# Kernel tuning notes

Measured on AMD Instinct MI355X. Metric: run time of the kernel, lower is better.

## Reference

```python
import jax, jax.numpy as jnp
import numpy as np

B, S, R, H = 256, 196, 1024, 512  # batch, att regions, rnn_size, att_hid_size


def setup_inputs() -> dict:
    key = jax.random.key(0)
    ks = jax.random.split(key, 8)
    return {
        "att_feats": jax.random.normal(ks[0], (B, S, R), dtype=jnp.float32),
        "p_att_feats": jax.random.normal(ks[1], (B, S, H), dtype=jnp.float32),
        "hidden": jax.random.normal(ks[2], (B, R), dtype=jnp.float32),
        "in_weights": jax.random.uniform(ks[3], (B, S), dtype=jnp.float32),
        "h2att_w": jax.random.normal(ks[4], (H, R), dtype=jnp.float32) * (1.0 / np.sqrt(R)),
        "h2att_b": jnp.full((H,), 0.1, dtype=jnp.float32),
        "alpha_w": jax.random.normal(ks[5], (1, H), dtype=jnp.float32) * (1.0 / np.sqrt(H)),
        "alpha_b": jnp.full((1,), 0.1, dtype=jnp.float32),
    }


def reference(att_feats, p_att_feats, hidden, in_weights, h2att_w, h2att_b, alpha_w, alpha_b):
    # att = in_weights * p_att_feats          [B, S, H]
    att = in_weights[:, :, None] * p_att_feats
    # att_h = h2att(hidden)                   [B, H] broadcast over S
    att_h = hidden @ h2att_w.T + h2att_b
    dot = jnp.tanh(att + att_h[:, None, :])   # [B, S, H]
    # alpha_net: Linear(H, 1) -> scores       [B, S]
    scores = jnp.einsum('bsh,h->bs', dot, alpha_w[0]) + alpha_b[0]
    weight = jax.nn.softmax(scores, axis=-1)  # [B, S]
    # weighted pooling: bmm(weight[:,None,:], att_feats).squeeze(1)
    att_res = jnp.einsum('bs,bsr->br', weight, att_feats)  # [B, R]
    return (att_res, weight)
```

## Files before the change

kernel.cpp:

```cpp
#include <hip/hip_runtime.h>
#include <math.h>

#define BN 256
#define SN 196
#define RN 1024
#define HN 512
#define KSPLIT 16
#define KCH 64

__device__ __forceinline__ float fast_tanh(float x) {
    float e = __expf(2.0f * x);
    return 1.0f - 2.0f * __builtin_amdgcn_rcpf(e + 1.0f);
}

__global__ __launch_bounds__(256) void k_gemm_partial(
    const float* __restrict__ hidden, const float* __restrict__ w,
    float* __restrict__ partial) {
    __shared__ float At[KCH][64];
    __shared__ float Bt[KCH][64];
    const int t  = threadIdx.x;
    const int b0 = blockIdx.x * 64;
    const int h0 = blockIdx.y * 64;
    const int kc = blockIdx.z;
    const int k0 = kc * KCH;

    {
        const int row = t >> 2, kq = (t & 3) * 16;
        const float* srcA = hidden + (size_t)(b0 + row) * RN + k0 + kq;
        const float* srcB = w      + (size_t)(h0 + row) * RN + k0 + kq;
#pragma unroll
        for (int j = 0; j < 4; ++j) {
            float4 v = *(const float4*)(srcA + j * 4);
            int k = kq + j * 4;
            At[k][row] = v.x; At[k + 1][row] = v.y; At[k + 2][row] = v.z; At[k + 3][row] = v.w;
        }
#pragma unroll
        for (int j = 0; j < 4; ++j) {
            float4 v = *(const float4*)(srcB + j * 4);
            int k = kq + j * 4;
            Bt[k][row] = v.x; Bt[k + 1][row] = v.y; Bt[k + 2][row] = v.z; Bt[k + 3][row] = v.w;
        }
    }
    __syncthreads();

    const int th4 = (t & 15) * 4;
    const int tb4 = (t >> 4) * 4;
    float4 acc0 = {0,0,0,0}, acc1 = {0,0,0,0}, acc2 = {0,0,0,0}, acc3 = {0,0,0,0};
#pragma unroll 8
    for (int k = 0; k < KCH; ++k) {
        float4 a  = *(const float4*)&At[k][tb4];
        float4 bb = *(const float4*)&Bt[k][th4];
        acc0.x = fmaf(a.x, bb.x, acc0.x); acc0.y = fmaf(a.x, bb.y, acc0.y);
        acc0.z = fmaf(a.x, bb.z, acc0.z); acc0.w = fmaf(a.x, bb.w, acc0.w);
        acc1.x = fmaf(a.y, bb.x, acc1.x); acc1.y = fmaf(a.y, bb.y, acc1.y);
        acc1.z = fmaf(a.y, bb.z, acc1.z); acc1.w = fmaf(a.y, bb.w, acc1.w);
        acc2.x = fmaf(a.z, bb.x, acc2.x); acc2.y = fmaf(a.z, bb.y, acc2.y);
        acc2.z = fmaf(a.z, bb.z, acc2.z); acc2.w = fmaf(a.z, bb.w, acc2.w);
        acc3.x = fmaf(a.w, bb.x, acc3.x); acc3.y = fmaf(a.w, bb.y, acc3.y);
        acc3.z = fmaf(a.w, bb.z, acc3.z); acc3.w = fmaf(a.w, bb.w, acc3.w);
    }
    float* dst = partial + ((size_t)kc * BN + b0 + tb4) * HN + h0 + th4;
    *(float4*)(dst)          = acc0;
    *(float4*)(dst + HN)     = acc1;
    *(float4*)(dst + 2 * HN) = acc2;
    *(float4*)(dst + 3 * HN) = acc3;
}

__global__ __launch_bounds__(1024) void k_fused(
    const float* __restrict__ partial, const float* __restrict__ bias,
    const float* __restrict__ p_att, const float* __restrict__ in_w,
    const float* __restrict__ alpha_w, const float* __restrict__ att_feats,
    float* __restrict__ att_res, float* __restrict__ weight_out) {
    __shared__ float att_h[HN];
    __shared__ float sc[256];
    __shared__ float red[16 * 256];
    const int b    = blockIdx.x;
    const int t    = threadIdx.x;
    const int wv   = t >> 6;
    const int lane = t & 63;

    if (t >= SN && t < 256) sc[t] = -1e30f;

    if (t < 128) {
        float4 s = *(const float4*)(bias + t * 4);
        const float* p = partial + (size_t)b * HN + t * 4;
#pragma unroll
        for (int kc = 0; kc < KSPLIT; ++kc) {
            float4 v = *(const float4*)(p + (size_t)kc * BN * HN);
            s.x += v.x; s.y += v.y; s.z += v.z; s.w += v.w;
        }
        *(float4*)&att_h[t * 4] = s;
    }
    __syncthreads();

    {
        const float4* a4 = (const float4*)alpha_w;
        float4 aw0 = a4[lane], aw1 = a4[lane + 64];
        float4 ah0 = *(const float4*)&att_h[lane * 4];
        float4 ah1 = *(const float4*)&att_h[(lane + 64) * 4];
        const float4* p4 = (const float4*)p_att;
        for (int si = wv; si < SN; si += 16) {
            float  iw = in_w[b * SN + si];
            size_t rb = (size_t)(b * SN + si) * (HN / 4);
            float4 p0 = p4[rb + lane];
            float4 p1 = p4[rb + lane + 64];
            float sum;
            sum  = fast_tanh(fmaf(iw, p0.x, ah0.x)) * aw0.x;
            sum += fast_tanh(fmaf(iw, p0.y, ah0.y)) * aw0.y;
            sum += fast_tanh(fmaf(iw, p0.z, ah0.z)) * aw0.z;
            sum += fast_tanh(fmaf(iw, p0.w, ah0.w)) * aw0.w;
            sum += fast_tanh(fmaf(iw, p1.x, ah1.x)) * aw1.x;
            sum += fast_tanh(fmaf(iw, p1.y, ah1.y)) * aw1.y;
            sum += fast_tanh(fmaf(iw, p1.z, ah1.z)) * aw1.z;
            sum += fast_tanh(fmaf(iw, p1.w, ah1.w)) * aw1.w;
#pragma unroll
            for (int off = 32; off; off >>= 1) sum += __shfl_xor(sum, off, 64);
            if (lane == 0) sc[si] = sum;
        }
    }
    __syncthreads();

    if (wv == 0) {
        float v0 = sc[lane], v1 = sc[lane + 64], v2 = sc[lane + 128], v3 = sc[lane + 192];
        float m = fmaxf(fmaxf(v0, v1), fmaxf(v2, v3));
#pragma unroll
        for (int off = 32; off; off >>= 1) m = fmaxf(m, __shfl_xor(m, off, 64));
        float e0 = __expf(v0 - m), e1 = __expf(v1 - m);
        float e2 = __expf(v2 - m), e3 = __expf(v3 - m);
        float s = e0 + e1 + e2 + e3;
#pragma unroll
        for (int off = 32; off; off >>= 1) s += __shfl_xor(s, off, 64);
        float inv = 1.0f / s;
        e0 *= inv; e1 *= inv; e2 *= inv; e3 *= inv;
        sc[lane] = e0; sc[lane + 64] = e1; sc[lane + 128] = e2; sc[lane + 192] = e3;
        float* wo = weight_out + (size_t)b * SN;
        wo[lane] = e0; wo[lane + 64] = e1; wo[lane + 128] = e2;
        if (lane + 192 < SN) wo[lane + 192] = e3;
    }
    __syncthreads();

    {
        const int g = wv >> 2, q = wv & 3;
        const float* base = att_feats + (size_t)b * SN * RN + q * 256 + lane * 4;
        float4 acc = {0,0,0,0};
        for (int i = 0; i < 49; i += 7) {
#pragma unroll
            for (int j = 0; j < 7; ++j) {
                int s = g + 4 * (i + j);
                float ws = sc[s];
                float4 v = *(const float4*)(base + (size_t)s * RN);
                acc.x = fmaf(ws, v.x, acc.x);
                acc.y = fmaf(ws, v.y, acc.y);
                acc.z = fmaf(ws, v.z, acc.z);
                acc.w = fmaf(ws, v.w, acc.w);
            }
        }
        *(float4*)&red[wv * 256 + lane * 4] = acc;
    }
    __syncthreads();
    {
        const int q2 = t >> 8, rr = t & 255;
        float r = red[q2 * 256 + rr] + red[(4 + q2) * 256 + rr]
                + red[(8 + q2) * 256 + rr] + red[(12 + q2) * 256 + rr];
        att_res[(size_t)b * RN + t] = r;
    }
}

extern "C" void kernel_launch(void* const* d_in, const int* in_sizes, int n_in,
                              void* d_out, int out_size, void* d_ws, size_t ws_size,
                              hipStream_t stream) {
    const float* att_feats   = (const float*)d_in[0];
    const float* p_att_feats = (const float*)d_in[1];
    const float* hidden      = (const float*)d_in[2];
    const float* in_weights  = (const float*)d_in[3];
    const float* h2att_w     = (const float*)d_in[4];
    const float* h2att_b     = (const float*)d_in[5];
    const float* alpha_w     = (const float*)d_in[6];

    float* att_res = (float*)d_out;
    float* weight  = (float*)d_out + BN * RN;
    float* partial = (float*)d_ws;

    k_gemm_partial<<<dim3(BN / 64, HN / 64, KSPLIT), 256, 0, stream>>>(
        hidden, h2att_w, partial);
    k_fused<<<BN, 1024, 0, stream>>>(partial, h2att_b, p_att_feats, in_weights,
                                     alpha_w, att_feats, att_res, weight);
}
```

Baseline: 363.0 us.

## Split fused attention kernel into separate reduce, scores, softmax and pool kernels

Replaces the single per-batch 1024-thread fused kernel with four kernels: a split-K reduction for att_h, a scores kernel with one wave per (batch, region) row, a softmax kernel, and a pooling kernel with two blocks per batch. The GEMM split-K factor is halved, and each GEMM block now loops over two 64-wide K sub-tiles. The aim is to spread the memory-bound p_att and att_feats streaming across many more blocks than the previous 256 large blocks. In exchange it adds kernel launches and round trips through global memory for att_h and the scores, and the pool kernel has only 512 small blocks.

```diff
diff --git a/kernel.cpp b/kernel.cpp
--- a/kernel.cpp
+++ b/kernel.cpp
@@ -5,8 +5,8 @@
 #define SN 196
 #define RN 1024
 #define HN 512
-#define KSPLIT 16
-#define KCH 64
+#define KSPLIT 8
+#define KCH 128
 
 __device__ __forceinline__ float fast_tanh(float x) {
     float e = __expf(2.0f * x);
@@ -16,48 +16,51 @@
 __global__ __launch_bounds__(256) void k_gemm_partial(
     const float* __restrict__ hidden, const float* __restrict__ w,
     float* __restrict__ partial) {
-    __shared__ float At[KCH][64];
-    __shared__ float Bt[KCH][64];
+    __shared__ float At[64][64];
+    __shared__ float Bt[64][64];
     const int t  = threadIdx.x;
     const int b0 = blockIdx.x * 64;
     const int h0 = blockIdx.y * 64;
     const int kc = blockIdx.z;
-    const int k0 = kc * KCH;
-
-    {
-        const int row = t >> 2, kq = (t & 3) * 16;
-        const float* srcA = hidden + (size_t)(b0 + row) * RN + k0 + kq;
-        const float* srcB = w      + (size_t)(h0 + row) * RN + k0 + kq;
-#pragma unroll
-        for (int j = 0; j < 4; ++j) {
-            float4 v = *(const float4*)(srcA + j * 4);
-            int k = kq + j * 4;
-            At[k][row] = v.x; At[k + 1][row] = v.y; At[k + 2][row] = v.z; At[k + 3][row] = v.w;
-        }
-#pragma unroll
-        for (int j = 0; j < 4; ++j) {
-            float4 v = *(const float4*)(srcB + j * 4);
-            int k = kq + j * 4;
-            Bt[k][row] = v.x; Bt[k + 1][row] = v.y; Bt[k + 2][row] = v.z; Bt[k + 3][row] = v.w;
-        }
-    }
-    __syncthreads();
 
     const int th4 = (t & 15) * 4;
     const int tb4 = (t >> 4) * 4;
     float4 acc0 = {0,0,0,0}, acc1 = {0,0,0,0}, acc2 = {0,0,0,0}, acc3 = {0,0,0,0};
+
+    for (int sub = 0; sub < 2; ++sub) {
+        const int k0 = kc * KCH + sub * 64;
+        {
+            const int row = t >> 2, kq = (t & 3) * 16;
+            const float* srcA = hidden + (size_t)(b0 + row) * RN + k0 + kq;
+            const float* srcB = w      + (size_t)(h0 + row) * RN + k0 + kq;
+#pragma unroll
+            for (int j = 0; j < 4; ++j) {
+                float4 v = *(const float4*)(srcA + j * 4);
+                int k = kq + j * 4;
+                At[k][row] = v.x; At[k+1][row] = v.y; At[k+2][row] = v.z; At[k+3][row] = v.w;
+            }
+#pragma unroll
+            for (int j = 0; j < 4; ++j) {
+                float4 v = *(const float4*)(srcB + j * 4);
+                int k = kq + j * 4;
+                Bt[k][row] = v.x; Bt[k+1][row] = v.y; Bt[k+2][row] = v.z; Bt[k+3][row] = v.w;
+            }
+        }
+        __syncthreads();
 #pragma unroll 8
-    for (int k = 0; k < KCH; ++k) {
-        float4 a  = *(const float4*)&At[k][tb4];
-        float4 bb = *(const float4*)&Bt[k][th4];
-        acc0.x = fmaf(a.x, bb.x, acc0.x); acc0.y = fmaf(a.x, bb.y, acc0.y);
-        acc0.z = fmaf(a.x, bb.z, acc0.z); acc0.w = fmaf(a.x, bb.w, acc0.w);
-        acc1.x = fmaf(a.y, bb.x, acc1.x); acc1.y = fmaf(a.y, bb.y, acc1.y);
-        acc1.z = fmaf(a.y, bb.z, acc1.z); acc1.w = fmaf(a.y, bb.w, acc1.w);
-        acc2.x = fmaf(a.z, bb.x, acc2.x); acc2.y = fmaf(a.z, bb.y, acc2.y);
-        acc2.z = fmaf(a.z, bb.z, acc2.z); acc2.w = fmaf(a.z, bb.w, acc2.w);
-        acc3.x = fmaf(a.w, bb.x, acc3.x); acc3.y = fmaf(a.w, bb.y, acc3.y);
-        acc3.z = fmaf(a.w, bb.z, acc3.z); acc3.w = fmaf(a.w, bb.w, acc3.w);
+        for (int k = 0; k < 64; ++k) {
+            float4 a  = *(const float4*)&At[k][tb4];
+            float4 bb = *(const float4*)&Bt[k][th4];
+            acc0.x = fmaf(a.x, bb.x, acc0.x); acc0.y = fmaf(a.x, bb.y, acc0.y);
+            acc0.z = fmaf(a.x, bb.z, acc0.z); acc0.w = fmaf(a.x, bb.w, acc0.w);
+            acc1.x = fmaf(a.y, bb.x, acc1.x); acc1.y = fmaf(a.y, bb.y, acc1.y);
+            acc1.z = fmaf(a.y, bb.z, acc1.z); acc1.w = fmaf(a.y, bb.w, acc1.w);
+            acc2.x = fmaf(a.z, bb.x, acc2.x); acc2.y = fmaf(a.z, bb.y, acc2.y);
+            acc2.z = fmaf(a.z, bb.z, acc2.z); acc2.w = fmaf(a.z, bb.w, acc2.w);
+            acc3.x = fmaf(a.w, bb.x, acc3.x); acc3.y = fmaf(a.w, bb.y, acc3.y);
+            acc3.z = fmaf(a.w, bb.z, acc3.z); acc3.w = fmaf(a.w, bb.w, acc3.w);
+        }
+        __syncthreads();
     }
     float* dst = partial + ((size_t)kc * BN + b0 + tb4) * HN + h0 + th4;
     *(float4*)(dst)          = acc0;
@@ -66,104 +69,111 @@
     *(float4*)(dst + 3 * HN) = acc3;
 }
 
-__global__ __launch_bounds__(1024) void k_fused(
+__global__ __launch_bounds__(128) void k_reduce(
     const float* __restrict__ partial, const float* __restrict__ bias,
+    float* __restrict__ att_h) {
+    const int b = blockIdx.x, t = threadIdx.x;
+    float4 s = *(const float4*)(bias + t * 4);
+    const float* p = partial + (size_t)b * HN + t * 4;
+#pragma unroll
+    for (int kc = 0; kc < KSPLIT; ++kc) {
+        float4 v = *(const float4*)(p + (size_t)kc * BN * HN);
+        s.x += v.x; s.y += v.y; s.z += v.z; s.w += v.w;
+    }
+    *(float4*)(att_h + (size_t)b * HN + t * 4) = s;
+}
+
+__global__ __launch_bounds__(256) void k_scores(
     const float* __restrict__ p_att, const float* __restrict__ in_w,
-    const float* __restrict__ alpha_w, const float* __restrict__ att_feats,
-    float* __restrict__ att_res, float* __restrict__ weight_out) {
-    __shared__ float att_h[HN];
-    __shared__ float sc[256];
-    __shared__ float red[16 * 256];
-    const int b    = blockIdx.x;
+    const float* __restrict__ att_h, const float* __restrict__ alpha_w,
+    float* __restrict__ scores) {
+    const int lane = threadIdx.x & 63;
+    const int gid  = blockIdx.x * 4 + (threadIdx.x >> 6);
+    const int b    = gid / SN;
+
+    const float iw = in_w[gid];
+    const float4* p4 = (const float4*)(p_att + (size_t)gid * HN);
+    const float4* a4 = (const float4*)(alpha_w);
+    const float4* h4 = (const float4*)(att_h + (size_t)b * HN);
+
+    float4 p0 = p4[lane], p1 = p4[lane + 64];
+    float4 aw0 = a4[lane], aw1 = a4[lane + 64];
+    float4 ah0 = h4[lane], ah1 = h4[lane + 64];
+
+    float sum;
+    sum  = fast_tanh(fmaf(iw, p0.x, ah0.x)) * aw0.x;
+    sum += fast_tanh(fmaf(iw, p0.y, ah0.y)) * aw0.y;
+    sum += fast_tanh(fmaf(iw, p0.z, ah0.z)) * aw0.z;
+    sum += fast_tanh(fmaf(iw, p0.w, ah0.w)) * aw0.w;
+    sum += fast_tanh(fmaf(iw, p1.x, ah1.x)) * aw1.x;
+    sum += fast_tanh(fmaf(iw, p1.y, ah1.y)) * aw1.y;
+    sum += fast_tanh(fmaf(iw, p1.z, ah1.z)) * aw1.z;
+    sum += fast_tanh(fmaf(iw, p1.w, ah1.w)) * aw1.w;
+#pragma unroll
+    for (int off = 32; off; off >>= 1) sum += __shfl_xor(sum, off, 64);
+    if (lane == 0) scores[gid] = sum;
+}
+
+__global__ __launch_bounds__(64) void k_softmax(float* __restrict__ wout) {
+    const int b = blockIdx.x, lane = threadIdx.x;
+    float* row = wout + (size_t)b * SN;
+
+    float v[4];
+    float m = -1e30f;
+#pragma unroll
+    for (int i = 0; i < 4; ++i) {
+        int s = lane + i * 64;
+        v[i] = (s < SN) ? row[s] : -1e30f;
+        m = fmaxf(m, v[i]);
+    }
+#pragma unroll
+    for (int off = 32; off; off >>= 1) m = fmaxf(m, __shfl_xor(m, off, 64));
+
+    float e[4];
+    float sum = 0.f;
+#pragma unroll
+    for (int i = 0; i < 4; ++i) {
+        int s = lane + i * 64;
+        e[i] = (s < SN) ? __expf(v[i] - m) : 0.f;
+        sum += e[i];
+    }
+#pragma unroll
+    for (int off = 32; off; off >>= 1) sum += __shfl_xor(sum, off, 64);
+
+    float inv = 1.0f / sum;
+#pragma unroll
+    for (int i = 0; i < 4; ++i) {
+        int s = lane + i * 64;
+        if (s < SN) row[s] = e[i] * inv;
+    }
+}
+
+__global__ __launch_bounds__(128) void k_pool(
+    const float* __restrict__ att_feats, const float* __restrict__ weight,
+    float* __restrict__ att_res) {
+    __shared__ float w[SN];
+    const int b    = blockIdx.x >> 1;
+    const int half = blockIdx.x & 1;
     const int t    = threadIdx.x;
-    const int wv   = t >> 6;
-    const int lane = t & 63;
-
-    if (t >= SN && t < 256) sc[t] = -1e30f;
-
-    if (t < 128) {
-        float4 s = *(const float4*)(bias + t * 4);
-        const float* p = partial + (size_t)b * HN + t * 4;
-#pragma unroll
-        for (int kc = 0; kc < KSPLIT; ++kc) {
-            float4 v = *(const float4*)(p + (size_t)kc * BN * HN);
-            s.x += v.x; s.y += v.y; s.z += v.z; s.w += v.w;
+
+    for (int s = t; s < SN; s += 128) w[s] = weight[(size_t)b * SN + s];
+    __syncthreads();
+
+    const float* base = att_feats + (size_t)b * SN * RN + half * 512 + t * 4;
+    float4 acc = {0, 0, 0, 0};
+    for (int i = 0; i < SN; i += 14) {
+#pragma unroll
+        for (int j = 0; j < 14; ++j) {
+            int s = i + j;
+            float ws = w[s];
+            float4 v = *(const float4*)(base + (size_t)s * RN);
+            acc.x = fmaf(ws, v.x, acc.x);
+            acc.y = fmaf(ws, v.y, acc.y);
+            acc.z = fmaf(ws, v.z, acc.z);
+            acc.w = fmaf(ws, v.w, acc.w);
         }
-        *(float4*)&att_h[t * 4] = s;
-    }
-    __syncthreads();
-
-    {
-        const float4* a4 = (const float4*)alpha_w;
-        float4 aw0 = a4[lane], aw1 = a4[lane + 64];
-        float4 ah0 = *(const float4*)&att_h[lane * 4];
-        float4 ah1 = *(const float4*)&att_h[(lane + 64) * 4];
-        const float4* p4 = (const float4*)p_att;
-        for (int si = wv; si < SN; si += 16) {
-            float  iw = in_w[b * SN + si];
-            size_t rb = (size_t)(b * SN + si) * (HN / 4);
-            float4 p0 = p4[rb + lane];
-            float4 p1 = p4[rb + lane + 64];
-            float sum;
-            sum  = fast_tanh(fmaf(iw, p0.x, ah0.x)) * aw0.x;
-            sum += fast_tanh(fmaf(iw, p0.y, ah0.y)) * aw0.y;
-            sum += fast_tanh(fmaf(iw, p0.z, ah0.z)) * aw0.z;
-            sum += fast_tanh(fmaf(iw, p0.w, ah0.w)) * aw0.w;
-            sum += fast_tanh(fmaf(iw, p1.x, ah1.x)) * aw1.x;
-            sum += fast_tanh(fmaf(iw, p1.y, ah1.y)) * aw1.y;
-            sum += fast_tanh(fmaf(iw, p1.z, ah1.z)) * aw1.z;
-            sum += fast_tanh(fmaf(iw, p1.w, ah1.w)) * aw1.w;
-#pragma unroll
-            for (int off = 32; off; off >>= 1) sum += __shfl_xor(sum, off, 64);
-            if (lane == 0) sc[si] = sum;
-        }
-    }
-    __syncthreads();
-
-    if (wv == 0) {
-        float v0 = sc[lane], v1 = sc[lane + 64], v2 = sc[lane + 128], v3 = sc[lane + 192];
-        float m = fmaxf(fmaxf(v0, v1), fmaxf(v2, v3));
-#pragma unroll
-        for (int off = 32; off; off >>= 1) m = fmaxf(m, __shfl_xor(m, off, 64));
-        float e0 = __expf(v0 - m), e1 = __expf(v1 - m);
-        float e2 = __expf(v2 - m), e3 = __expf(v3 - m);
-        float s = e0 + e1 + e2 + e3;
-#pragma unroll
-        for (int off = 32; off; off >>= 1) s += __shfl_xor(s, off, 64);
-        float inv = 1.0f / s;
-        e0 *= inv; e1 *= inv; e2 *= inv; e3 *= inv;
-        sc[lane] = e0; sc[lane + 64] = e1; sc[lane + 128] = e2; sc[lane + 192] = e3;
-        float* wo = weight_out + (size_t)b * SN;
-        wo[lane] = e0; wo[lane + 64] = e1; wo[lane + 128] = e2;
-        if (lane + 192 < SN) wo[lane + 192] = e3;
-    }
-    __syncthreads();
-
-    {
-        const int g = wv >> 2, q = wv & 3;
-        const float* base = att_feats + (size_t)b * SN * RN + q * 256 + lane * 4;
-        float4 acc = {0,0,0,0};
-        for (int i = 0; i < 49; i += 7) {
-#pragma unroll
-            for (int j = 0; j < 7; ++j) {
-                int s = g + 4 * (i + j);
-                float ws = sc[s];
-                float4 v = *(const float4*)(base + (size_t)s * RN);
-                acc.x = fmaf(ws, v.x, acc.x);
-                acc.y = fmaf(ws, v.y, acc.y);
-                acc.z = fmaf(ws, v.z, acc.z);
-                acc.w = fmaf(ws, v.w, acc.w);
-            }
-        }
-        *(float4*)&red[wv * 256 + lane * 4] = acc;
-    }
-    __syncthreads();
-    {
-        const int q2 = t >> 8, rr = t & 255;
-        float r = red[q2 * 256 + rr] + red[(4 + q2) * 256 + rr]
-                + red[(8 + q2) * 256 + rr] + red[(12 + q2) * 256 + rr];
-        att_res[(size_t)b * RN + t] = r;
-    }
+    }
+    *(float4*)(att_res + (size_t)b * RN + half * 512 + t * 4) = acc;
 }
 
 extern "C" void kernel_launch(void* const* d_in, const int* in_sizes, int n_in,
@@ -180,9 +190,11 @@
     float* att_res = (float*)d_out;
     float* weight  = (float*)d_out + BN * RN;
     float* partial = (float*)d_ws;
-
-    k_gemm_partial<<<dim3(BN / 64, HN / 64, KSPLIT), 256, 0, stream>>>(
-        hidden, h2att_w, partial);
-    k_fused<<<BN, 1024, 0, stream>>>(partial, h2att_b, p_att_feats, in_weights,
-                                     alpha_w, att_feats, att_res, weight);
-}
+    float* att_h   = (float*)d_ws + (size_t)KSPLIT * BN * HN;
+
+    k_gemm_partial<<<dim3(BN / 64, HN / 64, KSPLIT), 256, 0, stream>>>(hidden, h2att_w, partial);
+    k_reduce <<<BN, 128, 0, stream>>>(partial, h2att_b, att_h);
+    k_scores <<<(BN * SN) / 4, 256, 0, stream>>>(p_att_feats, in_weights, att_h, alpha_w, weight);
+    k_softmax<<<BN, 64, 0, stream>>>(weight);
+    k_pool   <<<BN * 2, 128, 0, stream>>>(att_feats, weight, att_res);
+}
```

Result: no change. 367.2 us (+1.2%).
